# Kernel optimization log

Hardware: AMD Instinct MI355X
Metric: run time of the kernel (lower is better)

Reference implementation:

```python
import jax, jax.numpy as jnp
import numpy as np

PATCH = 8
EMB = 16
SEQ = 130  # ceil(1039/8)
EPS = 1e-5


def _pos_encoding(seq_len, d_model):
    pos = jnp.arange(seq_len, dtype=jnp.float32)[:, None]
    div = jnp.exp(jnp.arange(0, d_model, 2, dtype=jnp.float32) * (-jnp.log(jnp.float32(10000.0)) / d_model))
    pe = jnp.zeros((seq_len, d_model), dtype=jnp.float32)
    pe = pe.at[:, 0::2].set(jnp.sin(pos * div))
    pe = pe.at[:, 1::2].set(jnp.cos(pos * div))
    return pe


def _layer_norm(x, g, b):
    m = x.mean(-1, keepdims=True)
    v = ((x - m) ** 2).mean(-1, keepdims=True)
    return (x - m) / jnp.sqrt(v + EPS) * g + b


def setup_inputs() -> dict:
    key = jax.random.key(0)
    ks = jax.random.split(key, 16)
    s = 0.1
    return {
        "x": jax.random.normal(ks[0], (8192, 1039), dtype=jnp.float32),
        "w_proj": jax.random.normal(ks[1], (EMB, PATCH), dtype=jnp.float32) * s,
        "b_proj": jax.random.normal(ks[2], (EMB,), dtype=jnp.float32) * s,
        "w_in": jax.random.normal(ks[3], (3 * EMB, EMB), dtype=jnp.float32) * s,
        "b_in": jax.random.normal(ks[4], (3 * EMB,), dtype=jnp.float32) * s,
        "w_out": jax.random.normal(ks[5], (EMB, EMB), dtype=jnp.float32) * s,
        "b_out": jax.random.normal(ks[6], (EMB,), dtype=jnp.float32) * s,
        "ln1_g": jnp.ones((EMB,), dtype=jnp.float32),
        "ln1_b": jnp.zeros((EMB,), dtype=jnp.float32),
        "w1": jax.random.normal(ks[7], (1, EMB), dtype=jnp.float32) * s,
        "b1": jax.random.normal(ks[8], (1,), dtype=jnp.float32) * s,
        "w2": jax.random.normal(ks[9], (EMB, 1), dtype=jnp.float32) * s,
        "b2": jax.random.normal(ks[10], (EMB,), dtype=jnp.float32) * s,
        "ln2_g": jnp.ones((EMB,), dtype=jnp.float32),
        "ln2_b": jnp.zeros((EMB,), dtype=jnp.float32),
    }


def reference(x, w_proj, b_proj, w_in, b_in, w_out, b_out,
              ln1_g, ln1_b, w1, b1, w2, b2, ln2_g, ln2_b):
    B, L = x.shape
    pad = (-L) % PATCH  # = 1 for L=1039
    xp = jnp.pad(x, ((0, 0), (0, pad)))
    patches = xp.reshape(B, -1, PATCH)                      # [B, S, 8]
    h = jnp.einsum('bsp,ep->bse', patches, w_proj) + b_proj  # [B, S, 16]
    h = h + _pos_encoding(h.shape[1], EMB)

    # single-head self-attention (dropout=0 at eval)
    qkv = jnp.einsum('bse,fe->bsf', h, w_in) + b_in          # [B, S, 48]
    q, k, v = jnp.split(qkv, 3, axis=-1)
    scale = 1.0 / jnp.sqrt(jnp.float32(EMB))
    scores = jnp.einsum('bqe,bke->bqk', q, k) * scale        # [B, S, S]
    attn = jax.nn.softmax(scores, axis=-1)
    ctx = jnp.einsum('bqk,bke->bqe', attn, v)
    attn_out = jnp.einsum('bse,fe->bsf', ctx, w_out) + b_out

    h = _layer_norm(h + attn_out, ln1_g, ln1_b)

    ff = jax.nn.relu(jnp.einsum('bse,fe->bsf', h, w1) + b1)  # [B, S, 1]
    ff = jnp.einsum('bsf,ef->bse', ff, w2) + b2              # [B, S, 16]
    h = _layer_norm(h + ff, ln2_g, ln2_b)

    return h.mean(axis=1)  # [B, 16]
```

## Files before the change

### kernel.cpp

```cpp
#include <hip/hip_runtime.h>
#include <math.h>

#define SEQ 130
#define EMB 16
#define LIN 1039
#define NB 2
#define WPB 4

typedef __attribute__((ext_vector_type(4))) _Float16 half4v;
typedef __attribute__((ext_vector_type(4))) float float4v;

__global__ void pe_kernel(const float* __restrict__ b_proj, float* __restrict__ pe2) {
    int idx = blockIdx.x * 256 + threadIdx.x;
    if (idx < 144 * 16) {
        int s = idx >> 4, e = idx & 15;
        float v = 0.f;
        if (s < SEQ) {
            int i = e >> 1;
            float div = expf(-(float)(2 * i) * 0.57564627324851149f);
            float ang = (float)s * div;
            v = ((e & 1) ? cosf(ang) : sinf(ang)) + b_proj[e];
        }
        pe2[idx] = v;
    }
}

__global__ __launch_bounds__(256) void st_kernel(
    const float* __restrict__ x,
    const float* __restrict__ w_proj,
    const float* __restrict__ w_in,  const float* __restrict__ b_in,
    const float* __restrict__ w_out, const float* __restrict__ b_out,
    const float* __restrict__ ln1_g, const float* __restrict__ ln1_b,
    const float* __restrict__ w1,    const float* __restrict__ b1,
    const float* __restrict__ w2,    const float* __restrict__ b2,
    const float* __restrict__ ln2_g, const float* __restrict__ ln2_b,
    const float* __restrict__ pe2,
    int nbat,
    float* __restrict__ out)
{
    const int tid  = threadIdx.x;
    const int lane = tid & 63;
    const int c    = lane & 15;
    const int g    = lane >> 4;
    const int wgid = blockIdx.x * WPB + (tid >> 6);
    const float4v zero4 = {0.f, 0.f, 0.f, 0.f};

    half4v wprojF, wqF, wkF, wvF, woF;
    {
        #pragma unroll
        for (int j = 0; j < 4; ++j)
            wprojF[j] = (_Float16)((g < 2) ? w_proj[c * 8 + 4 * g + j] : 0.f);
        const float* pq = &w_in[c * 16 + 4 * g];
        const float* pk = &w_in[(16 + c) * 16 + 4 * g];
        const float* pv = &w_in[(32 + c) * 16 + 4 * g];
        const float* po = &w_out[c * 16 + 4 * g];
        #pragma unroll
        for (int j = 0; j < 4; ++j) {
            wqF[j] = (_Float16)(pq[j] * 0.25f);
            wkF[j] = (_Float16)pk[j];
            wvF[j] = (_Float16)pv[j];
            woF[j] = (_Float16)po[j];
        }
    }
    half4v bqH, bkH, boH, g1H, b1H, g2H, b2H, w1H, w2H, bb2H;
    #pragma unroll
    for (int j = 0; j < 4; ++j) {
        const int f = 4 * g + j;
        bqH[j]  = (_Float16)(b_in[f] * 0.25f);
        bkH[j]  = (_Float16)b_in[16 + f];
        boH[j]  = (_Float16)b_out[f];
        g1H[j]  = (_Float16)ln1_g[f];  b1H[j]  = (_Float16)ln1_b[f];
        g2H[j]  = (_Float16)ln2_g[f];  b2H[j]  = (_Float16)ln2_b[f];
        w1H[j]  = (_Float16)w1[f];     w2H[j]  = (_Float16)w2[f];
        bb2H[j] = (_Float16)b2[f];
    }
    const float bvc = b_in[32 + c];
    const float b1v = b1[0];

    for (int bi = 0; bi < NB; ++bi) {
        const int batch = wgid * NB + bi;
        if (batch >= nbat) break;
        const float* xrow = x + (size_t)batch * LIN;

        half4v hf[9];
        #pragma unroll
        for (int st = 0; st < 9; ++st) {
            const int s = st * 16 + c;
            half4v xf;
            if (st < 8) {
                if (g < 2) {
                    const float* xp = &xrow[s * 8 + 4 * g];
                    #pragma unroll
                    for (int j = 0; j < 4; ++j) xf[j] = (_Float16)xp[j];
                } else {
                    #pragma unroll
                    for (int j = 0; j < 4; ++j) xf[j] = (_Float16)0.f;
                }
            } else {
                #pragma unroll
                for (int j = 0; j < 4; ++j) {
                    const int idx = s * 8 + 4 * g + j;
                    const float v = (g < 2 && idx < LIN) ? xrow[idx] : 0.f;
                    xf[j] = (_Float16)v;
                }
            }
            float4v d = __builtin_amdgcn_mfma_f32_16x16x16f16(wprojF, xf, zero4, 0, 0, 0);
            const float* pp = &pe2[s * 16 + 4 * g];
            #pragma unroll
            for (int j = 0; j < 4; ++j) hf[st][j] = (_Float16)(d[j] + pp[j]);
        }

        half4v kf[9], vf[9];
        #pragma unroll
        for (int st = 0; st < 9; ++st) {
            float4v dk = __builtin_amdgcn_mfma_f32_16x16x16f16(wkF, hf[st], zero4, 0, 0, 0);
            float4v dv = __builtin_amdgcn_mfma_f32_16x16x16f16(hf[st], wvF, zero4, 0, 0, 0);
            #pragma unroll
            for (int j = 0; j < 4; ++j) {
                kf[st][j] = (_Float16)(dk[j] + (float)bkH[j]);
                vf[st][j] = (_Float16)(dv[j] + bvc);
            }
        }

        float accm[4] = {0.f, 0.f, 0.f, 0.f};
        #pragma unroll
        for (int p = 0; p < 5; ++p) {
            const int nt = (p < 4) ? 2 : 1;
            half4v qf[2];
            float4v Oa[2], Ob[2];
            float l[2];
            #pragma unroll
            for (int u = 0; u < 2; ++u) if (u < nt) {
                const int ti = 2 * p + u;
                float4v dq = __builtin_amdgcn_mfma_f32_16x16x16f16(wqF, hf[ti], zero4, 0, 0, 0);
                #pragma unroll
                for (int j = 0; j < 4; ++j) qf[u][j] = (_Float16)(dq[j] + (float)bqH[j]);
                Oa[u] = zero4; Ob[u] = zero4; l[u] = 0.f;
            }
            #pragma unroll
            for (int kt = 0; kt < 9; ++kt) {
                #pragma unroll
                for (int u = 0; u < 2; ++u) if (u < nt) {
                    float4v s4 = __builtin_amdgcn_mfma_f32_16x16x16f16(kf[kt], qf[u], zero4, 0, 0, 0);
                    float p0 = __expf(s4[0]), p1 = __expf(s4[1]);
                    float p2 = __expf(s4[2]), p3 = __expf(s4[3]);
                    if (kt == 8) {
                        p2 = 0.f; p3 = 0.f;
                        if (g > 0) { p0 = 0.f; p1 = 0.f; }
                    }
                    l[u] += (p0 + p1) + (p2 + p3);
                    half4v pf = {(_Float16)p0, (_Float16)p1, (_Float16)p2, (_Float16)p3};
                    if (kt & 1) Ob[u] = __builtin_amdgcn_mfma_f32_16x16x16f16(vf[kt], pf, Ob[u], 0, 0, 0);
                    else        Oa[u] = __builtin_amdgcn_mfma_f32_16x16x16f16(vf[kt], pf, Oa[u], 0, 0, 0);
                }
            }
            #pragma unroll
            for (int u = 0; u < 2; ++u) if (u < nt) l[u] += __shfl_xor(l[u], 16);
            #pragma unroll
            for (int u = 0; u < 2; ++u) if (u < nt) l[u] += __shfl_xor(l[u], 32);
            #pragma unroll
            for (int u = 0; u < 2; ++u) if (u < nt) {
                const int ti = 2 * p + u;
                half4v cf;
                #pragma unroll
                for (int j = 0; j < 4; ++j) cf[j] = (_Float16)(Oa[u][j] + Ob[u][j]);
                float4v AO = __builtin_amdgcn_mfma_f32_16x16x16f16(woF, cf, zero4, 0, 0, 0);
                const float inv = __builtin_amdgcn_rcpf(l[u]);
                float h2[4];
                #pragma unroll
                for (int j = 0; j < 4; ++j)
                    h2[j] = (float)hf[ti][j] + AO[j] * inv + (float)boH[j];
                float s1 = (h2[0] + h2[1]) + (h2[2] + h2[3]);
                float q1 = (h2[0]*h2[0] + h2[1]*h2[1]) + (h2[2]*h2[2] + h2[3]*h2[3]);
                s1 += __shfl_xor(s1, 16); q1 += __shfl_xor(q1, 16);
                s1 += __shfl_xor(s1, 32); q1 += __shfl_xor(q1, 32);
                const float mean = s1 * 0.0625f;
                const float rstd = __builtin_amdgcn_rsqf(
                    q1 * 0.0625f - mean * mean + 1e-5f);
                #pragma unroll
                for (int j = 0; j < 4; ++j)
                    h2[j] = (h2[j] - mean) * rstd * (float)g1H[j] + (float)b1H[j];
                float fa = h2[0] * (float)w1H[0] + h2[1] * (float)w1H[1]
                         + h2[2] * (float)w1H[2] + h2[3] * (float)w1H[3];
                fa += __shfl_xor(fa, 16); fa += __shfl_xor(fa, 32);
                const float ffa = fmaxf(fa + b1v, 0.f);
                #pragma unroll
                for (int j = 0; j < 4; ++j)
                    h2[j] += ffa * (float)w2H[j] + (float)bb2H[j];
                float s2 = (h2[0] + h2[1]) + (h2[2] + h2[3]);
                float q2 = (h2[0]*h2[0] + h2[1]*h2[1]) + (h2[2]*h2[2] + h2[3]*h2[3]);
                s2 += __shfl_xor(s2, 16); q2 += __shfl_xor(q2, 16);
                s2 += __shfl_xor(s2, 32); q2 += __shfl_xor(q2, 32);
                const float mean2 = s2 * 0.0625f;
                const float rstd2 = __builtin_amdgcn_rsqf(
                    q2 * 0.0625f - mean2 * mean2 + 1e-5f);
                if (ti < 8 || c < 2) {
                    #pragma unroll
                    for (int j = 0; j < 4; ++j)
                        accm[j] += (h2[j] - mean2) * rstd2 * (float)g2H[j] + (float)b2H[j];
                }
            }
        }

        #pragma unroll
        for (int off = 1; off < 16; off <<= 1) {
            #pragma unroll
            for (int j = 0; j < 4; ++j) accm[j] += __shfl_xor(accm[j], off);
        }
        if (c == 0) {
            float* op = &out[(size_t)batch * 16 + 4 * g];
            #pragma unroll
            for (int j = 0; j < 4; ++j) op[j] = accm[j] * (1.0f / 130.0f);
        }
    }
}

extern "C" void kernel_launch(void* const* d_in, const int* in_sizes, int n_in,
                              void* d_out, int out_size, void* d_ws, size_t ws_size,
                              hipStream_t stream) {
    const float* x      = (const float*)d_in[0];
    const float* w_proj = (const float*)d_in[1];
    const float* b_proj = (const float*)d_in[2];
    const float* w_in   = (const float*)d_in[3];
    const float* b_in   = (const float*)d_in[4];
    const float* w_out  = (const float*)d_in[5];
    const float* b_out  = (const float*)d_in[6];
    const float* ln1_g  = (const float*)d_in[7];
    const float* ln1_b  = (const float*)d_in[8];
    const float* w1     = (const float*)d_in[9];
    const float* b1     = (const float*)d_in[10];
    const float* w2     = (const float*)d_in[11];
    const float* b2     = (const float*)d_in[12];
    const float* ln2_g  = (const float*)d_in[13];
    const float* ln2_b  = (const float*)d_in[14];

    float* pe2 = (float*)d_ws;
    pe_kernel<<<9, 256, 0, stream>>>(b_proj, pe2);

    int B = in_sizes[0] / LIN;
    int grid = (B + WPB * NB - 1) / (WPB * NB);
    st_kernel<<<grid, 256, 0, stream>>>(x, w_proj, w_in, b_in,
                                        w_out, b_out, ln1_g, ln1_b,
                                        w1, b1, w2, b2, ln2_g, ln2_b,
                                        pe2, B, (float*)d_out);
}
```

Measured before the change: 75.26 us.

## Fold biases into MFMA accumulators and do LayerNorm/FFN reductions via MFMA

Initializes the patch-projection MFMA accumulator with the positional-encoding+bias vector and the K-projection accumulator with the K bias, removing separate adds. Replaces the cross-lane shuffle reductions in both LayerNorms and the FFN dot product with MFMA calls against a ones matrix or the w1 vector, so that row sums come out broadcast in the accumulator. This trades DPP/shuffle latency for extra MFMA instructions. It also computes squares and sums in fp16 inputs, which loses precision in the variance.

```diff
diff --git a/kernel.cpp b/kernel.cpp
--- a/kernel.cpp
+++ b/kernel.cpp
@@ -45,7 +45,7 @@
     const int wgid = blockIdx.x * WPB + (tid >> 6);
     const float4v zero4 = {0.f, 0.f, 0.f, 0.f};
 
-    half4v wprojF, wqF, wkF, wvF, woF;
+    half4v wprojF, wqF, wkF, wvF, woF, onesF;
     {
         #pragma unroll
         for (int j = 0; j < 4; ++j)
@@ -60,14 +60,16 @@
             wkF[j] = (_Float16)pk[j];
             wvF[j] = (_Float16)pv[j];
             woF[j] = (_Float16)po[j];
-        }
-    }
-    half4v bqH, bkH, boH, g1H, b1H, g2H, b2H, w1H, w2H, bb2H;
+            onesF[j] = (_Float16)1.0f;
+        }
+    }
+    float4v bkC4;
+    half4v bqH, boH, g1H, b1H, g2H, b2H, w1H, w2H, bb2H;
     #pragma unroll
     for (int j = 0; j < 4; ++j) {
         const int f = 4 * g + j;
+        bkC4[j] = b_in[16 + f];
         bqH[j]  = (_Float16)(b_in[f] * 0.25f);
-        bkH[j]  = (_Float16)b_in[16 + f];
         boH[j]  = (_Float16)b_out[f];
         g1H[j]  = (_Float16)ln1_g[f];  b1H[j]  = (_Float16)ln1_b[f];
         g2H[j]  = (_Float16)ln2_g[f];  b2H[j]  = (_Float16)ln2_b[f];
@@ -104,20 +106,20 @@
                     xf[j] = (_Float16)v;
                 }
             }
-            float4v d = __builtin_amdgcn_mfma_f32_16x16x16f16(wprojF, xf, zero4, 0, 0, 0);
-            const float* pp = &pe2[s * 16 + 4 * g];
-            #pragma unroll
-            for (int j = 0; j < 4; ++j) hf[st][j] = (_Float16)(d[j] + pp[j]);
+            const float4v pe4 = *(const float4v*)&pe2[s * 16 + 4 * g];
+            float4v d = __builtin_amdgcn_mfma_f32_16x16x16f16(wprojF, xf, pe4, 0, 0, 0);
+            #pragma unroll
+            for (int j = 0; j < 4; ++j) hf[st][j] = (_Float16)d[j];
         }
 
         half4v kf[9], vf[9];
         #pragma unroll
         for (int st = 0; st < 9; ++st) {
-            float4v dk = __builtin_amdgcn_mfma_f32_16x16x16f16(wkF, hf[st], zero4, 0, 0, 0);
+            float4v dk = __builtin_amdgcn_mfma_f32_16x16x16f16(wkF, hf[st], bkC4, 0, 0, 0);
             float4v dv = __builtin_amdgcn_mfma_f32_16x16x16f16(hf[st], wvF, zero4, 0, 0, 0);
             #pragma unroll
             for (int j = 0; j < 4; ++j) {
-                kf[st][j] = (_Float16)(dk[j] + (float)bkH[j]);
+                kf[st][j] = (_Float16)dk[j];
                 vf[st][j] = (_Float16)(dv[j] + bvc);
             }
         }
@@ -167,33 +169,38 @@
                 float4v AO = __builtin_amdgcn_mfma_f32_16x16x16f16(woF, cf, zero4, 0, 0, 0);
                 const float inv = __builtin_amdgcn_rcpf(l[u]);
                 float h2[4];
-                #pragma unroll
-                for (int j = 0; j < 4; ++j)
+                half4v h2f, hqf;
+                #pragma unroll
+                for (int j = 0; j < 4; ++j) {
                     h2[j] = (float)hf[ti][j] + AO[j] * inv + (float)boH[j];
-                float s1 = (h2[0] + h2[1]) + (h2[2] + h2[3]);
-                float q1 = (h2[0]*h2[0] + h2[1]*h2[1]) + (h2[2]*h2[2] + h2[3]*h2[3]);
-                s1 += __shfl_xor(s1, 16); q1 += __shfl_xor(q1, 16);
-                s1 += __shfl_xor(s1, 32); q1 += __shfl_xor(q1, 32);
-                const float mean = s1 * 0.0625f;
+                    h2f[j] = (_Float16)h2[j];
+                    hqf[j] = (_Float16)(h2[j] * h2[j]);
+                }
+                float4v SM = __builtin_amdgcn_mfma_f32_16x16x16f16(onesF, h2f, zero4, 0, 0, 0);
+                float4v SQ = __builtin_amdgcn_mfma_f32_16x16x16f16(onesF, hqf, zero4, 0, 0, 0);
+                const float mean = SM[0] * 0.0625f;
                 const float rstd = __builtin_amdgcn_rsqf(
-                    q1 * 0.0625f - mean * mean + 1e-5f);
-                #pragma unroll
-                for (int j = 0; j < 4; ++j)
+                    SQ[0] * 0.0625f - mean * mean + 1e-5f);
+                half4v h2nf;
+                #pragma unroll
+                for (int j = 0; j < 4; ++j) {
                     h2[j] = (h2[j] - mean) * rstd * (float)g1H[j] + (float)b1H[j];
-                float fa = h2[0] * (float)w1H[0] + h2[1] * (float)w1H[1]
-                         + h2[2] * (float)w1H[2] + h2[3] * (float)w1H[3];
-                fa += __shfl_xor(fa, 16); fa += __shfl_xor(fa, 32);
-                const float ffa = fmaxf(fa + b1v, 0.f);
-                #pragma unroll
-                for (int j = 0; j < 4; ++j)
+                    h2nf[j] = (_Float16)h2[j];
+                }
+                float4v FA = __builtin_amdgcn_mfma_f32_16x16x16f16(w1H, h2nf, zero4, 0, 0, 0);
+                const float ffa = fmaxf(FA[0] + b1v, 0.f);
+                half4v h3f, h3qf;
+                #pragma unroll
+                for (int j = 0; j < 4; ++j) {
                     h2[j] += ffa * (float)w2H[j] + (float)bb2H[j];
-                float s2 = (h2[0] + h2[1]) + (h2[2] + h2[3]);
-                float q2 = (h2[0]*h2[0] + h2[1]*h2[1]) + (h2[2]*h2[2] + h2[3]*h2[3]);
-                s2 += __shfl_xor(s2, 16); q2 += __shfl_xor(q2, 16);
-                s2 += __shfl_xor(s2, 32); q2 += __shfl_xor(q2, 32);
-                const float mean2 = s2 * 0.0625f;
+                    h3f[j]  = (_Float16)h2[j];
+                    h3qf[j] = (_Float16)(h2[j] * h2[j]);
+                }
+                float4v SM2 = __builtin_amdgcn_mfma_f32_16x16x16f16(onesF, h3f, zero4, 0, 0, 0);
+                float4v SQ2 = __builtin_amdgcn_mfma_f32_16x16x16f16(onesF, h3qf, zero4, 0, 0, 0);
+                const float mean2 = SM2[0] * 0.0625f;
                 const float rstd2 = __builtin_amdgcn_rsqf(
-                    q2 * 0.0625f - mean2 * mean2 + 1e-5f);
+                    SQ2[0] * 0.0625f - mean2 * mean2 + 1e-5f);
                 if (ti < 8 || c < 2) {
                     #pragma unroll
                     for (int j = 0; j < 4; ++j)
```

Result: slower. 99.14 us (+31.7%).
